# Kernel tuning notes

Measured on AMD Instinct MI355X. Metric: run time of the kernel, lower is better.

The kernel has to match this reference:

```python
import math
import jax, jax.numpy as jnp
import numpy as np

N_HEADS = 8

def setup_inputs() -> dict:
    key = jax.random.key(0)
    qkv = jax.random.normal(key, (4, 3 * N_HEADS * 64, 2048), dtype=jnp.float32)
    return {"qkv": qkv}

def reference(qkv) -> jnp.ndarray:
    bs, width, length = qkv.shape
    assert width % (3 * N_HEADS) == 0
    ch = width // (3 * N_HEADS)
    q, k, v = jnp.split(qkv, 3, axis=1)            # each [N, H*C, T]
    scale = 1.0 / math.sqrt(math.sqrt(ch))
    qh = (q * scale).reshape(bs * N_HEADS, ch, length)  # [BH, C, T]
    kh = (k * scale).reshape(bs * N_HEADS, ch, length)
    vh = v.reshape(bs * N_HEADS, ch, length)
    weight = jnp.einsum('bct,bcs->bts', qh, kh)    # [BH, T, T]
    weight = jax.nn.softmax(weight.astype(jnp.float32), axis=-1).astype(weight.dtype)
    a = jnp.einsum('bts,bcs->bct', weight, vh)     # [BH, C, T]
    return a.reshape(bs, -1, length)
```

## Files before the change

### kernel.cpp

```cpp
#include <hip/hip_runtime.h>
#include <math.h>

#define T_LEN 2048
#define CH 64
#define NH 8
#define STILE 64
#define TTILE 128
#define WT 32
#define NIT (T_LEN / STILE)
#define CSK 68
#define CS 72
#define PS2 40
#define QS 132
#define RS 68

#define QSCALE 0.180336880972948929f

typedef __attribute__((ext_vector_type(4))) float  f32x4;
typedef __attribute__((ext_vector_type(8))) __bf16 bf16x8;
typedef __attribute__((ext_vector_type(4))) __bf16 bf16x4;

union SMem {
  float qstage[CH * QS];
  struct {
    __bf16 k_hi[2][STILE * CSK];
    __bf16 v_s [3][CH * CS];
    __bf16 p_s [8 * WT * PS2];
  } loop;
  struct {
    float o[4][WT][RS];
    float l[4][2][4][16];
  } red;
};

#define MFMA(A, B, C) __builtin_amdgcn_mfma_f32_16x16x32_bf16((A), (B), (C), 0, 0, 0)

__device__ __forceinline__ void load_k(const float* kp, int s0, int tid, float2 (&kreg)[4]) {
  int cq  = tid >> 5;
  int sp2 = tid & 31;
  const float* kc = kp + (size_t)(4 * cq) * T_LEN + s0 + 2 * sp2;
#pragma unroll
  for (int r = 0; r < 4; ++r)
    kreg[r] = *(const float2*)(kc + (size_t)r * T_LEN);
}

__device__ __forceinline__ void store_k(__bf16* kh, int tid, const float2 (&kreg)[4]) {
  int cq  = tid >> 5;
  int sp2 = tid & 31;
  bf16x4 w0 = {(__bf16)kreg[0].x, (__bf16)kreg[1].x, (__bf16)kreg[2].x, (__bf16)kreg[3].x};
  bf16x4 w1 = {(__bf16)kreg[0].y, (__bf16)kreg[1].y, (__bf16)kreg[2].y, (__bf16)kreg[3].y};
  *(bf16x4*)&kh[(2 * sp2 + 0) * CSK + 4 * cq] = w0;
  *(bf16x4*)&kh[(2 * sp2 + 1) * CSK + 4 * cq] = w1;
}

__device__ __forceinline__ void load_v(const float* vp, int s0, int tid, f32x4 (&vreg)[2]) {
#pragma unroll
  for (int rr = 0; rr < 2; ++rr) {
    int fidx = rr * 512 + tid;
    int c  = fidx >> 4;
    int s4 = (fidx & 15) << 2;
    vreg[rr] = *(const f32x4*)(vp + (size_t)c * T_LEN + s0 + s4);
  }
}

__device__ __forceinline__ void store_v(__bf16* vs, int tid, const f32x4 (&vreg)[2]) {
#pragma unroll
  for (int rr = 0; rr < 2; ++rr) {
    int fidx = rr * 512 + tid;
    int c  = fidx >> 4;
    int s4 = (fidx & 15) << 2;
    bf16x4 vv = {(__bf16)vreg[rr].x, (__bf16)vreg[rr].y,
                 (__bf16)vreg[rr].z, (__bf16)vreg[rr].w};
    *(bf16x4*)&vs[c * CS + s4] = vv;
  }
}

__global__ __launch_bounds__(512, 4)
void qkv_attn_mfma(const float* __restrict__ qkv, float* __restrict__ out) {
  __shared__ SMem sm;
  const int tid  = threadIdx.x;
  const int lane = tid & 63;
  const int wave = tid >> 6;
  const int wt   = wave & 3;
  const int ws   = wave >> 2;
  const int tn   = lane & 15;
  const int quad = lane >> 4;

  const int ttile = blockIdx.x;
  const int bh    = blockIdx.y;
  const int b = bh >> 3, h = bh & 7;
  const size_t base = (size_t)b * (3 * NH * CH) * T_LEN;
  const float* qp = qkv + base + (size_t)(CH * h) * T_LEN;
  const float* kp = qkv + base + (size_t)(CH * (NH + h)) * T_LEN;
  const float* vp = qkv + base + (size_t)(CH * (2 * NH + h)) * T_LEN;
  const int t0 = ttile * TTILE;

#pragma unroll
  for (int rr = 0; rr < 4; ++rr) {
    int fidx = rr * 512 + tid;
    int c  = fidx >> 5;
    int t4 = (fidx & 31) << 2;
    f32x4 q4 = *(const f32x4*)(qp + (size_t)c * T_LEN + t0 + t4);
    *(f32x4*)&sm.qstage[c * QS + t4] = q4;
  }
  __syncthreads();

  bf16x8 qh[2][2];
#pragma unroll
  for (int nb = 0; nb < 2; ++nb)
#pragma unroll
    for (int kb = 0; kb < 2; ++kb) {
      int tloc = wt * WT + nb * 16 + tn;
      bf16x8 H;
#pragma unroll
      for (int j = 0; j < 8; ++j) {
        float qv = sm.qstage[(kb * 32 + quad * 8 + j) * QS + tloc] * QSCALE;
        H[j] = (__bf16)qv;
      }
      qh[nb][kb] = H;
    }
  __syncthreads();

  f32x4 acc[4][2];
  float l_part[2] = {0.f, 0.f};
#pragma unroll
  for (int mbc = 0; mbc < 4; ++mbc)
#pragma unroll
    for (int nb = 0; nb < 2; ++nb)
      acc[mbc][nb] = (f32x4){0.f, 0.f, 0.f, 0.f};

  __bf16* pw = &sm.loop.p_s[wave * (WT * PS2)];

  float2 kreg[4];
  f32x4  vreg[2];
  load_k(kp, 0, tid, kreg);
  load_v(vp, 0, tid, vreg);
  store_k(sm.loop.k_hi[0], tid, kreg);
  store_v(sm.loop.v_s[0], tid, vreg);
  __syncthreads();

  int vrd = 2, vwr = 1;

  for (int it = 0; it < NIT; ++it) {
    const int kcur = it & 1;
    const bool more = (it + 1 < NIT);

    if (it > 0) {
      bf16x8 bp[2];
#pragma unroll
      for (int nb = 0; nb < 2; ++nb)
        bp[nb] = *(const bf16x8*)&pw[(nb * 16 + tn) * PS2 + quad * 8];
      bf16x8 av[4];
      const __bf16* vs = sm.loop.v_s[vrd];
#pragma unroll
      for (int mbc = 0; mbc < 4; ++mbc)
        av[mbc] = *(const bf16x8*)&vs[(16 * mbc + tn) * CS + 32 * ws + quad * 8];
#pragma unroll
      for (int mbc = 0; mbc < 4; ++mbc)
#pragma unroll
        for (int nb = 0; nb < 2; ++nb)
          acc[mbc][nb] = MFMA(av[mbc], bp[nb], acc[mbc][nb]);
    }

    if (more) {
      load_k(kp, (it + 1) * STILE, tid, kreg);
      load_v(vp, (it + 1) * STILE, tid, vreg);
    }

    const __bf16* kh = sm.loop.k_hi[kcur];
    bf16x8 ah[2][2];
#pragma unroll
    for (int mb = 0; mb < 2; ++mb) {
      const int srow = (32 * ws + 16 * mb + tn) * CSK;
#pragma unroll
      for (int kb = 0; kb < 2; ++kb) {
        bf16x4 a0 = *(const bf16x4*)&kh[srow + 32 * kb + quad * 8];
        bf16x4 a1 = *(const bf16x4*)&kh[srow + 32 * kb + quad * 8 + 4];
        ah[mb][kb] = __builtin_shufflevector(a0, a1, 0, 1, 2, 3, 4, 5, 6, 7);
      }
    }
    f32x4 d[2][2];
#pragma unroll
    for (int mb = 0; mb < 2; ++mb)
#pragma unroll
      for (int nb = 0; nb < 2; ++nb) {
        f32x4 t = (f32x4){0.f, 0.f, 0.f, 0.f};
        t = MFMA(ah[mb][0], qh[nb][0], t);
        t = MFMA(ah[mb][1], qh[nb][1], t);
        d[mb][nb] = t;
      }

#pragma unroll
    for (int nb = 0; nb < 2; ++nb) {
      float rs = 0.f;
#pragma unroll
      for (int mb = 0; mb < 2; ++mb)
#pragma unroll
        for (int r = 0; r < 4; ++r) {
          float e = __builtin_amdgcn_exp2f(d[mb][nb][r]);
          d[mb][nb][r] = e;
          rs += e;
        }
      l_part[nb] += rs;
    }

    asm volatile("" ::: "memory");

#pragma unroll
    for (int nb = 0; nb < 2; ++nb)
#pragma unroll
      for (int mb = 0; mb < 2; ++mb) {
        f32x4 pv4 = d[mb][nb];
        bf16x4 pb = {(__bf16)pv4.x, (__bf16)pv4.y, (__bf16)pv4.z, (__bf16)pv4.w};
        *(bf16x4*)&pw[(nb * 16 + tn) * PS2 + mb * 16 + quad * 4] = pb;
      }

    if (more) {
      store_k(sm.loop.k_hi[kcur ^ 1], tid, kreg);
      store_v(sm.loop.v_s[vwr], tid, vreg);
    }
    vrd = (vrd == 2) ? 0 : vrd + 1;
    vwr = (vwr == 2) ? 0 : vwr + 1;
    __syncthreads();
  }

  {
    bf16x8 bp[2];
#pragma unroll
    for (int nb = 0; nb < 2; ++nb)
      bp[nb] = *(const bf16x8*)&pw[(nb * 16 + tn) * PS2 + quad * 8];
    bf16x8 av[4];
    const __bf16* vs = sm.loop.v_s[vrd];
#pragma unroll
    for (int mbc = 0; mbc < 4; ++mbc)
      av[mbc] = *(const bf16x8*)&vs[(16 * mbc + tn) * CS + 32 * ws + quad * 8];
#pragma unroll
    for (int mbc = 0; mbc < 4; ++mbc)
#pragma unroll
      for (int nb = 0; nb < 2; ++nb)
        acc[mbc][nb] = MFMA(av[mbc], bp[nb], acc[mbc][nb]);
  }
  __syncthreads();

  if (ws == 1) {
#pragma unroll
    for (int nb = 0; nb < 2; ++nb) {
      sm.red.l[wt][nb][quad][tn] = l_part[nb];
#pragma unroll
      for (int mbc = 0; mbc < 4; ++mbc)
        *(f32x4*)&sm.red.o[wt][nb * 16 + tn][16 * mbc + quad * 4] = acc[mbc][nb];
    }
  }
  __syncthreads();
  if (ws == 0) {
    float* op = out + (size_t)bh * CH * T_LEN;
#pragma unroll
    for (int nb = 0; nb < 2; ++nb) {
      float l = l_part[nb] + sm.red.l[wt][nb][quad][tn];
      l += __shfl_xor(l, 16, 64);
      l += __shfl_xor(l, 32, 64);
      float inv_l = 1.0f / l;
      int t = t0 + wt * WT + nb * 16 + tn;
#pragma unroll
      for (int mbc = 0; mbc < 4; ++mbc) {
        f32x4 o = acc[mbc][nb] + *(const f32x4*)&sm.red.o[wt][nb * 16 + tn][16 * mbc + quad * 4];
        o = o * inv_l;
        int c = 16 * mbc + quad * 4;
        op[(size_t)(c + 0) * T_LEN + t] = o.x;
        op[(size_t)(c + 1) * T_LEN + t] = o.y;
        op[(size_t)(c + 2) * T_LEN + t] = o.z;
        op[(size_t)(c + 3) * T_LEN + t] = o.w;
      }
    }
  }
}

extern "C" void kernel_launch(void* const* d_in, const int* in_sizes, int n_in,
                              void* d_out, int out_size, void* d_ws, size_t ws_size,
                              hipStream_t stream) {
  const float* qkv = (const float*)d_in[0];
  float* out = (float*)d_out;
  dim3 grid(T_LEN / TTILE, 32);
  qkv_attn_mfma<<<grid, 512, 0, stream>>>(qkv, out);
}
```

Measured before the change: 129.3 us.

## Shrink LDS buffering and raise occupancy target with single K buffer

Replaces the double-buffered K tile and triple-buffered V tile with a single K buffer and a double V buffer. This cuts shared memory per block so more blocks can be resident, and raises the launch-bounds occupancy hint from 4 to 6. Next-tile global loads are issued at the top of each iteration, and K is now loaded with scalar per-lane strided accesses instead of float2. The single K buffer needs an extra __syncthreads per iteration before the next K is stored. The tighter register budget may cause spills, and the grid already fits on the device at the old occupancy.

Measured after the change: 232.2 us. 79.6% more time.

```diff
diff --git a/kernel.cpp b/kernel.cpp
--- a/kernel.cpp
+++ b/kernel.cpp
@@ -23,9 +23,9 @@
 union SMem {
   float qstage[CH * QS];
   struct {
-    __bf16 k_hi[2][STILE * CSK];
-    __bf16 v_s [3][CH * CS];
-    __bf16 p_s [8 * WT * PS2];
+    __bf16 k_s[STILE * CSK];
+    __bf16 v_s[2][CH * CS];
+    __bf16 p_s[8 * WT * PS2];
   } loop;
   struct {
     float o[4][WT][RS];
@@ -36,21 +36,23 @@
 #define MFMA(A, B, C) __builtin_amdgcn_mfma_f32_16x16x32_bf16((A), (B), (C), 0, 0, 0)
 
 __device__ __forceinline__ void load_k(const float* kp, int s0, int tid, float2 (&kreg)[4]) {
-  int cq  = tid >> 5;
-  int sp2 = tid & 31;
-  const float* kc = kp + (size_t)(4 * cq) * T_LEN + s0 + 2 * sp2;
-#pragma unroll
-  for (int r = 0; r < 4; ++r)
-    kreg[r] = *(const float2*)(kc + (size_t)r * T_LEN);
+  int cq = tid >> 5;
+  int sp = tid & 31;
+  const float* kc = kp + (size_t)(4 * cq) * T_LEN + s0 + sp;
+#pragma unroll
+  for (int r = 0; r < 4; ++r) {
+    kreg[r].x = kc[(size_t)r * T_LEN];
+    kreg[r].y = kc[(size_t)r * T_LEN + 32];
+  }
 }
 
 __device__ __forceinline__ void store_k(__bf16* kh, int tid, const float2 (&kreg)[4]) {
-  int cq  = tid >> 5;
-  int sp2 = tid & 31;
+  int cq = tid >> 5;
+  int sp = tid & 31;
   bf16x4 w0 = {(__bf16)kreg[0].x, (__bf16)kreg[1].x, (__bf16)kreg[2].x, (__bf16)kreg[3].x};
   bf16x4 w1 = {(__bf16)kreg[0].y, (__bf16)kreg[1].y, (__bf16)kreg[2].y, (__bf16)kreg[3].y};
-  *(bf16x4*)&kh[(2 * sp2 + 0) * CSK + 4 * cq] = w0;
-  *(bf16x4*)&kh[(2 * sp2 + 1) * CSK + 4 * cq] = w1;
+  *(bf16x4*)&kh[(sp +  0) * CSK + 4 * cq] = w0;
+  *(bf16x4*)&kh[(sp + 32) * CSK + 4 * cq] = w1;
 }
 
 __device__ __forceinline__ void load_v(const float* vp, int s0, int tid, f32x4 (&vreg)[2]) {
@@ -75,7 +77,7 @@
   }
 }
 
-__global__ __launch_bounds__(512, 4)
+__global__ __launch_bounds__(512, 6)
 void qkv_attn_mfma(const float* __restrict__ qkv, float* __restrict__ out) {
   __shared__ SMem sm;
   const int tid  = threadIdx.x;
@@ -135,23 +137,25 @@
   f32x4  vreg[2];
   load_k(kp, 0, tid, kreg);
   load_v(vp, 0, tid, vreg);
-  store_k(sm.loop.k_hi[0], tid, kreg);
+  store_k(sm.loop.k_s, tid, kreg);
   store_v(sm.loop.v_s[0], tid, vreg);
   __syncthreads();
 
-  int vrd = 2, vwr = 1;
-
   for (int it = 0; it < NIT; ++it) {
-    const int kcur = it & 1;
     const bool more = (it + 1 < NIT);
 
+    if (more) {
+      load_k(kp, (it + 1) * STILE, tid, kreg);
+      load_v(vp, (it + 1) * STILE, tid, vreg);
+    }
+
     if (it > 0) {
+      const __bf16* vs = sm.loop.v_s[(it - 1) & 1];
       bf16x8 bp[2];
 #pragma unroll
       for (int nb = 0; nb < 2; ++nb)
         bp[nb] = *(const bf16x8*)&pw[(nb * 16 + tn) * PS2 + quad * 8];
       bf16x8 av[4];
-      const __bf16* vs = sm.loop.v_s[vrd];
 #pragma unroll
       for (int mbc = 0; mbc < 4; ++mbc)
         av[mbc] = *(const bf16x8*)&vs[(16 * mbc + tn) * CS + 32 * ws + quad * 8];
@@ -162,20 +166,14 @@
           acc[mbc][nb] = MFMA(av[mbc], bp[nb], acc[mbc][nb]);
     }
 
-    if (more) {
-      load_k(kp, (it + 1) * STILE, tid, kreg);
-      load_v(vp, (it + 1) * STILE, tid, vreg);
-    }
-
-    const __bf16* kh = sm.loop.k_hi[kcur];
     bf16x8 ah[2][2];
 #pragma unroll
     for (int mb = 0; mb < 2; ++mb) {
       const int srow = (32 * ws + 16 * mb + tn) * CSK;
 #pragma unroll
       for (int kb = 0; kb < 2; ++kb) {
-        bf16x4 a0 = *(const bf16x4*)&kh[srow + 32 * kb + quad * 8];
-        bf16x4 a1 = *(const bf16x4*)&kh[srow + 32 * kb + quad * 8 + 4];
+        bf16x4 a0 = *(const bf16x4*)&sm.loop.k_s[srow + 32 * kb + quad * 8];
+        bf16x4 a1 = *(const bf16x4*)&sm.loop.k_s[srow + 32 * kb + quad * 8 + 4];
         ah[mb][kb] = __builtin_shufflevector(a0, a1, 0, 1, 2, 3, 4, 5, 6, 7);
       }
     }
@@ -215,22 +213,22 @@
         *(bf16x4*)&pw[(nb * 16 + tn) * PS2 + mb * 16 + quad * 4] = pb;
       }
 
+    __syncthreads();
+
     if (more) {
-      store_k(sm.loop.k_hi[kcur ^ 1], tid, kreg);
-      store_v(sm.loop.v_s[vwr], tid, vreg);
-    }
-    vrd = (vrd == 2) ? 0 : vrd + 1;
-    vwr = (vwr == 2) ? 0 : vwr + 1;
+      store_k(sm.loop.k_s, tid, kreg);
+      store_v(sm.loop.v_s[(it + 1) & 1], tid, vreg);
+    }
     __syncthreads();
   }
 
   {
+    const __bf16* vs = sm.loop.v_s[(NIT - 1) & 1];
     bf16x8 bp[2];
 #pragma unroll
     for (int nb = 0; nb < 2; ++nb)
       bp[nb] = *(const bf16x8*)&pw[(nb * 16 + tn) * PS2 + quad * 8];
     bf16x8 av[4];
-    const __bf16* vs = sm.loop.v_s[vrd];
 #pragma unroll
     for (int mbc = 0; mbc < 4; ++mbc)
       av[mbc] = *(const bf16x8*)&vs[(16 * mbc + tn) * CS + 32 * ws + quad * 8];
```
